# Optimization experiments

Measured on AMD Instinct MI355X. Metric: run time of the kernel, lower is better.

Reference implementation:

```python
import jax, jax.numpy as jnp
import numpy as np

B = 1024      # batch
HG = 28       # grid side (28x28 image -> graph)
N = HG * HG   # 784 nodes per sample
K = 70        # node_sampled (relaxed categorical classes)
GCN_OUT = 48
H_DIM = 400
Z = 70
IMG = 784
TEMP = 0.5


def _grid_edges():
    idx = np.arange(N).reshape(HG, HG)
    src = np.concatenate([idx[:, :-1].ravel(), idx[:, 1:].ravel(), idx[:-1, :].ravel(), idx[1:, :].ravel()])
    dst = np.concatenate([idx[:, 1:].ravel(), idx[:, :-1].ravel(), idx[1:, :].ravel(), idx[:-1, :].ravel()])
    loop = np.arange(N)
    return (np.concatenate([src, loop]).astype(np.int32),
            np.concatenate([dst, loop]).astype(np.int32))


def _lin(key, fi, fo):
    kw, kb = jax.random.split(key)
    s = 1.0 / np.sqrt(fi)
    return (jax.random.uniform(kw, (fi, fo), jnp.float32, -s, s),
            jax.random.uniform(kb, (fo,), jnp.float32, -s, s))


def setup_inputs() -> dict:
    key = jax.random.key(0)
    ks = jax.random.split(key, 16)
    src, dst = _grid_edges()
    u = jax.random.uniform(ks[2], (B, N, K), jnp.float32, 1e-6, 1.0 - 1e-6)
    inp = {
        'nodes': jax.random.normal(ks[0], (B, N, 2), jnp.float32),
        'logits': jax.random.normal(ks[1], (B, N, K), jnp.float32),
        'gumbel': -jnp.log(-jnp.log(u)),
        'eps': jax.random.normal(ks[3], (B, Z), jnp.float32),
    }
    inp['W1'], inp['b1'] = _lin(ks[4], 2, 16)
    inp['W2'], inp['b2'] = _lin(ks[5], 16, 32)
    inp['W3'], inp['b3'] = _lin(ks[6], 32, GCN_OUT)
    inp['We1'], inp['be1'] = _lin(ks[7], K * GCN_OUT, H_DIM)
    inp['We2'], inp['be2'] = _lin(ks[8], H_DIM, H_DIM)
    inp['Wmu'], inp['bmu'] = _lin(ks[9], H_DIM, Z)
    inp['Wvar'], inp['bvar'] = _lin(ks[10], H_DIM, Z)
    inp['Wd1'], inp['bd1'] = _lin(ks[11], Z, H_DIM)
    inp['Wd2'], inp['bd2'] = _lin(ks[12], H_DIM, IMG)
    inp['edge_src'] = jnp.asarray(src)
    inp['edge_dst'] = jnp.asarray(dst)
    return inp


def reference(nodes, logits, gumbel, eps,
              W1, b1, W2, b2, W3, b3,
              We1, be1, We2, be2,
              Wmu, bmu, Wvar, bvar,
              Wd1, bd1, Wd2, bd2,
              edge_src, edge_dst):
    # symmetric GCN normalization with self loops (already in edge list)
    deg = jnp.zeros((N,), nodes.dtype).at[edge_dst].add(1.0)
    dinv = jax.lax.rsqrt(deg)
    norm = dinv[edge_src] * dinv[edge_dst]  # [E]

    def gcn(h, W, b):
        h = h @ W                                   # [B,N,Fout]
        msg = h[:, edge_src] * norm[None, :, None]  # gather + scale, [B,E,Fout]
        return jnp.zeros_like(h).at[:, edge_dst].add(msg) + b

    h = jax.nn.relu(gcn(nodes, W1, b1))
    h = jax.nn.relu(gcn(h, W2, b2))
    h = jax.nn.relu(gcn(h, W3, b3))            # [B,N,48]

    # RelaxedOneHotCategorical(temp=0.5).rsample() == gumbel-softmax
    sample = jax.nn.softmax((logits + gumbel) / TEMP, axis=-1)  # [B,N,K]
    g = jnp.einsum('bnk,bnf->bkf', sample, h).reshape(h.shape[0], K * GCN_OUT)

    # encoder MLP + reparameterize
    e = jax.nn.relu(g @ We1 + be1)
    e = jax.nn.relu(e @ We2 + be2)
    mu = e @ Wmu + bmu
    var = jax.nn.softplus(e @ Wvar + bvar)
    z = mu + eps * jnp.sqrt(var + 1e-10)

    # decoder
    d = jax.nn.relu(z @ Wd1 + bd1)
    x_rec = jax.nn.sigmoid(d @ Wd2 + bd2)      # [B,784]
    return x_rec
```

## Files before the change

### kernel.cpp

```cpp
#include <hip/hip_runtime.h>
#include <hip/hip_bf16.h>


#define BB 1024
#define HG 28
#define NN 784
#define KK 70
#define F3 48
#define HD 400
#define ZD 70
#define IMGD 784

typedef __hip_bfloat16 bf16;
typedef __attribute__((ext_vector_type(8))) short s8v;
typedef __attribute__((ext_vector_type(4))) float f32x4;

__device__ __forceinline__ float dinv_ij(int i, int j){
  int deg = 1 + (i>0) + (i<HG-1) + (j>0) + (j<HG-1);
  return rsqrtf((float)deg);
}

__device__ __forceinline__ unsigned pk2(float a, float b){
  union { bf16 h; unsigned short u; } ua, ub;
  ua.h = __float2bfloat16(a); ub.h = __float2bfloat16(b);
  return ((unsigned)ub.u << 16) | ua.u;
}

__device__ __forceinline__ short bfbits(float v){
  union { bf16 h; short s; } u; u.h = __float2bfloat16(v); return u.s;
}

__global__ __launch_bounds__(256, 2)
void gcn_fused(const float* __restrict__ nodes,
               const float* __restrict__ W1, const float* __restrict__ b1,
               const float* __restrict__ W2, const float* __restrict__ b2,
               const float* __restrict__ W3, const float* __restrict__ b3,
               bf16* __restrict__ h3){
  __shared__ __align__(16) char smem[73216];
  float* regA = (float*)smem;
  float* regB = (float*)(smem + 36288);
  float* wbuf = (float*)(smem + 64512);
  float* W1s = wbuf;          float* b1s = wbuf + 32;
  float* W2s = wbuf + 48;     float* b2s = wbuf + 560;
  float* W3s = wbuf + 592;    float* b3s = wbuf + 2128;

  int tid = threadIdx.x;
  if (tid < 32)  W1s[tid] = W1[tid];
  if (tid < 16)  b1s[tid] = b1[tid];
  for (int t = tid; t < 512;  t += 256) W2s[t] = W2[t];
  if (tid < 32)  b2s[tid] = b2[tid];
  for (int t = tid; t < 1536; t += 256) W3s[t] = W3[t];
  if (tid < 48)  b3s[tid] = b3[tid];

  int b = blockIdx.x >> 2, s = blockIdx.x & 3;
  int base3 = s*7;
  int base2 = base3 - 1;
  int base1 = base3 - 2;
  const float* nb = nodes + (size_t)b*NN*2;
  __syncthreads();

  {
    float* h1s = regA;
    for (int t = tid; t < 308; t += 256){
      int lr = t/28, j = t - lr*28;
      int r = base1 + lr;
      float o[16] __attribute__((aligned(16)));
      if (r < 0 || r >= HG){
        #pragma unroll
        for (int f=0; f<16; f++) o[f] = 0.f;
      } else {
        float dn = dinv_ij(r,j);
        float a0 = dn*nb[(r*HG+j)*2+0], a1 = dn*nb[(r*HG+j)*2+1];
        if (r > 0)   { float w=dinv_ij(r-1,j); a0 += w*nb[((r-1)*HG+j)*2]; a1 += w*nb[((r-1)*HG+j)*2+1]; }
        if (r < HG-1){ float w=dinv_ij(r+1,j); a0 += w*nb[((r+1)*HG+j)*2]; a1 += w*nb[((r+1)*HG+j)*2+1]; }
        if (j > 0)   { float w=dinv_ij(r,j-1); a0 += w*nb[(r*HG+j-1)*2];   a1 += w*nb[(r*HG+j-1)*2+1]; }
        if (j < HG-1){ float w=dinv_ij(r,j+1); a0 += w*nb[(r*HG+j+1)*2];   a1 += w*nb[(r*HG+j+1)*2+1]; }
        a0 *= dn; a1 *= dn;
        #pragma unroll
        for (int f=0; f<16; f++) o[f] = fmaxf(a0*W1s[f] + a1*W1s[16+f] + b1s[f], 0.f);
      }
      float* dst = h1s + t*20;
      #pragma unroll
      for (int q=0; q<4; q++) *(float4*)(dst + 4*q) = *(float4*)&o[4*q];
    }
  }
  __syncthreads();

  if (tid < 252){
    const float* h1s = regA;
    float* agg1 = regB;
    int lr = tid/28, j = tid - lr*28;
    int r = base2 + lr;
    float o[16] __attribute__((aligned(16)));
    if (r < 0 || r >= HG){
      #pragma unroll
      for (int f=0; f<16; f++) o[f] = 0.f;
    } else {
      int ln = (lr+1)*28 + j;
      float dn = dinv_ij(r,j);
      float wu = dinv_ij(r-1,j), wd = dinv_ij(r+1,j);
      float wl = (j>0)    ? dinv_ij(r,j-1) : 0.f;
      float wr = (j<HG-1) ? dinv_ij(r,j+1) : 0.f;
      const float* pc = h1s + ln*20;
      #pragma unroll
      for (int q=0; q<4; q++){
        float4 vc = *(const float4*)(pc + 4*q);
        float4 vu = *(const float4*)(pc - 28*20 + 4*q);
        float4 vd = *(const float4*)(pc + 28*20 + 4*q);
        float4 vl = *(const float4*)(pc - 20 + 4*q);
        float4 vr = *(const float4*)(pc + 20 + 4*q);
        o[4*q+0] = dn*(dn*vc.x + wu*vu.x + wd*vd.x + wl*vl.x + wr*vr.x);
        o[4*q+1] = dn*(dn*vc.y + wu*vu.y + wd*vd.y + wl*vl.y + wr*vr.y);
        o[4*q+2] = dn*(dn*vc.z + wu*vu.z + wd*vd.z + wl*vl.z + wr*vr.z);
        o[4*q+3] = dn*(dn*vc.w + wu*vu.w + wd*vd.w + wl*vl.w + wr*vr.w);
      }
    }
    float* dst = agg1 + tid*20;
    #pragma unroll
    for (int q=0; q<4; q++) *(float4*)(dst + 4*q) = *(float4*)&o[4*q];
  }
  __syncthreads();

  {
    const float* agg1 = regB;
    float* h2s = regA;
    int tx = tid & 7, ty = tid >> 3;
    float4 w2r[16];
    #pragma unroll
    for (int fi=0; fi<16; fi++) w2r[fi] = *(const float4*)&W2s[fi*32 + tx*4];
    float4 bb = *(const float4*)&b2s[tx*4];
    #pragma unroll
    for (int i=0; i<8; i++){
      int n = ty + 32*i;
      if (n < 252){
        float af[16] __attribute__((aligned(16)));
        const float* ap = agg1 + n*20;
        #pragma unroll
        for (int q=0; q<4; q++) *(float4*)&af[4*q] = *(const float4*)(ap + 4*q);
        float4 acc = bb;
        #pragma unroll
        for (int fi=0; fi<16; fi++){
          float a = af[fi];
          acc.x += a*w2r[fi].x; acc.y += a*w2r[fi].y;
          acc.z += a*w2r[fi].z; acc.w += a*w2r[fi].w;
        }
        acc.x = fmaxf(acc.x,0.f); acc.y = fmaxf(acc.y,0.f);
        acc.z = fmaxf(acc.z,0.f); acc.w = fmaxf(acc.w,0.f);
        *(float4*)&h2s[n*36 + tx*4] = acc;
      }
    }
  }
  __syncthreads();

  if (tid < 196){
    const float* h2s = regA;
    float* agg2 = regB;
    int lr = tid/28, j = tid - lr*28;
    int r = base3 + lr;
    int ln = (lr+1)*28 + j;
    float dn = dinv_ij(r,j);
    float wu = dinv_ij(r-1,j), wd = dinv_ij(r+1,j);
    float wl = (j>0)    ? dinv_ij(r,j-1) : 0.f;
    float wr = (j<HG-1) ? dinv_ij(r,j+1) : 0.f;
    const float* pc = h2s + ln*36;
    float* dst = agg2 + tid*36;
    #pragma unroll
    for (int q=0; q<8; q++){
      float4 vc = *(const float4*)(pc + 4*q);
      float4 vu = *(const float4*)(pc - 28*36 + 4*q);
      float4 vd = *(const float4*)(pc + 28*36 + 4*q);
      float4 vl = *(const float4*)(pc - 36 + 4*q);
      float4 vr = *(const float4*)(pc + 36 + 4*q);
      float4 o;
      o.x = dn*(dn*vc.x + wu*vu.x + wd*vd.x + wl*vl.x + wr*vr.x);
      o.y = dn*(dn*vc.y + wu*vu.y + wd*vd.y + wl*vl.y + wr*vr.y);
      o.z = dn*(dn*vc.z + wu*vu.z + wd*vd.z + wl*vl.z + wr*vr.z);
      o.w = dn*(dn*vc.w + wu*vu.w + wd*vd.w + wl*vl.w + wr*vr.w);
      *(float4*)(dst + 4*q) = o;
    }
  }
  __syncthreads();

  {
    bf16* h3buf = (bf16*)regA;
    if (tid < 252){
      const float* agg2 = regB;
      int tx = tid % 12, ty = tid / 12;
      float4 w3r[32];
      #pragma unroll
      for (int fi=0; fi<32; fi++) w3r[fi] = *(const float4*)&W3s[fi*48 + tx*4];
      float4 bb = *(const float4*)&b3s[tx*4];
      #pragma unroll
      for (int i=0; i<10; i++){
        int n = ty + 21*i;
        if (n < 196){
          float af[32] __attribute__((aligned(16)));
          const float* ap = agg2 + n*36;
          #pragma unroll
          for (int q=0; q<8; q++) *(float4*)&af[4*q] = *(const float4*)(ap + 4*q);
          float4 acc = bb;
          #pragma unroll
          for (int fi=0; fi<32; fi++){
            float a = af[fi];
            acc.x += a*w3r[fi].x; acc.y += a*w3r[fi].y;
            acc.z += a*w3r[fi].z; acc.w += a*w3r[fi].w;
          }
          uint2 pv;
          pv.x = pk2(fmaxf(acc.x,0.f), fmaxf(acc.y,0.f));
          pv.y = pk2(fmaxf(acc.z,0.f), fmaxf(acc.w,0.f));
          *(uint2*)((char*)h3buf + n*112 + tx*8) = pv;
        }
      }
    }
  }
  __syncthreads();

  {
    const char* h3buf = (const char*)regA;
    uint4* dst = (uint4*)(h3 + ((size_t)b*NN + base3*28)*F3);
    for (int t = tid; t < 1176; t += 256){
      int n = t/6, gq = t - n*6;
      dst[t] = *(const uint4*)(h3buf + n*112 + gq*16);
    }
  }
}

__global__ __launch_bounds__(256)
void einsum_mfma_kernel(const float* __restrict__ logits, const float* __restrict__ gumbel,
                        const bf16* __restrict__ h3, float* __restrict__ g){
  __shared__ __align__(16) char smem[47872];
  float* samp = (float*)smem;
  short* stp  = (short*)(smem + 17920);
  short* stlo = (short*)(smem + 29440);
  short* htp  = (short*)(smem + 40960);
  float* cred = (float*)smem;

  int b = blockIdx.x;
  int tid = threadIdx.x;
  int l = tid & 63, w = tid >> 6;
  int ks = w >> 1, mh = w & 1;
  int mtoff = mh ? 3 : 0, mtcnt = mh ? 2 : 3;
  int nl = tid >> 2, q = tid & 3;
  int st = (q < 2) ? q*18 : 36 + (q-2)*17;
  int cnt = (q < 2) ? 18 : 17;

  f32x4 acc[3][3];
  #pragma unroll
  for (int mt=0; mt<3; mt++)
    #pragma unroll
    for (int bt=0; bt<3; bt++) acc[mt][bt] = (f32x4){0.f,0.f,0.f,0.f};

  float4 xs[5];
  uint4 hv[2];

  auto do_loads = [&](int c){
    int c0 = c*64;
    int nv = (c == 12) ? 16 : 64;
    int lim4 = nv*70/4, limh = nv*6;
    const float4* l4 = (const float4*)(logits + ((size_t)b*NN + c0)*KK);
    const float4* g4 = (const float4*)(gumbel + ((size_t)b*NN + c0)*KK);
    #pragma unroll
    for (int s=0; s<5; s++){
      int t = tid + s*256;
      if (t < lim4){
        float4 lv = l4[t], gv = g4[t];
        xs[s] = (float4){2.f*(lv.x+gv.x), 2.f*(lv.y+gv.y), 2.f*(lv.z+gv.z), 2.f*(lv.w+gv.w)};
      } else xs[s] = (float4){0.f,0.f,0.f,0.f};
    }
    const uint4* h4 = (const uint4*)(h3 + ((size_t)b*NN + c0)*F3);
    #pragma unroll
    for (int s=0; s<2; s++){
      int t = tid + s*256;
      hv[s] = (t < limh) ? h4[t] : (uint4){0u,0u,0u,0u};
    }
  };

  auto write_samp = [&](){
    #pragma unroll
    for (int s=0; s<5; s++){
      int t = tid + s*256;
      if (t < 1120) ((float4*)samp)[t] = xs[s];
    }
  };

  auto softmax_writes = [&](int c){
    int nv = (c == 12) ? 16 : 64;
    float p[18];
    if (nl < nv){
      float x[18];
      float m = -1e30f;
      #pragma unroll
      for (int i=0; i<18; i++) if (i < cnt){ x[i] = samp[nl*70 + st + i]; m = fmaxf(m, x[i]); }
      m = fmaxf(m, __shfl_xor(m, 1));
      m = fmaxf(m, __shfl_xor(m, 2));
      float sum = 0.f;
      #pragma unroll
      for (int i=0; i<18; i++) if (i < cnt){ x[i] = __expf(x[i]-m); sum += x[i]; }
      sum += __shfl_xor(sum, 1);
      sum += __shfl_xor(sum, 2);
      float r = 1.0f/sum;
      #pragma unroll
      for (int i=0; i<18; i++) p[i] = x[i]*r;
    } else {
      #pragma unroll
      for (int i=0; i<18; i++) p[i] = 0.f;
    }
    #pragma unroll
    for (int i=0; i<18; i++) if (i < cnt){
      int k = st + i;
      short hi = bfbits(p[i]);
      union { short s; bf16 h; } uh; uh.s = hi;
      float lo = p[i] - __bfloat162float(uh.h);
      stp[k*72 + nl]  = hi;
      stlo[k*72 + nl] = bfbits(lo);
    }
    #pragma unroll
    for (int s=0; s<2; s++){
      int t = tid + s*256;
      if (t < 384){
        int n = t/6, j = t - n*6, f0 = j*8;
        unsigned vv[4] = {hv[s].x, hv[s].y, hv[s].z, hv[s].w};
        #pragma unroll
        for (int i2=0; i2<4; i2++){
          htp[(f0+2*i2  )*72 + n] = (short)(vv[i2] & 0xFFFFu);
          htp[(f0+2*i2+1)*72 + n] = (short)(vv[i2] >> 16);
        }
      }
    }
  };

  auto do_mfma = [&](){
    int n0 = ks*32 + (l>>4)*8;
    #pragma unroll
    for (int bt=0; bt<3; bt++){
      s8v bfr = *(const s8v*)&htp[(bt*16 + (l&15))*72 + n0];
      #pragma unroll
      for (int mt=0; mt<3; mt++) if (mt < mtcnt){
        int row = (mtoff + mt)*16 + (l&15);
        s8v ah = *(const s8v*)&stp[row*72 + n0];
        s8v al = *(const s8v*)&stlo[row*72 + n0];
        acc[mt][bt] = __builtin_amdgcn_mfma_f32_16x16x32_bf16(ah, bfr, acc[mt][bt], 0, 0, 0);
        acc[mt][bt] = __builtin_amdgcn_mfma_f32_16x16x32_bf16(al, bfr, acc[mt][bt], 0, 0, 0);
      }
    }
  };

  do_loads(0);
  write_samp();
  __syncthreads();
  softmax_writes(0);
  __syncthreads();

  for (int c = 0; c < 13; c++){
    if (c < 12) do_loads(c+1);
    do_mfma();
    if (c < 12) write_samp();
    __syncthreads();
    if (c < 12){
      softmax_writes(c+1);
      __syncthreads();
    }
  }

  if (ks == 0){
    #pragma unroll
    for (int mt=0; mt<3; mt++) if (mt < mtcnt)
      #pragma unroll
      for (int bt=0; bt<3; bt++)
        #pragma unroll
        for (int r=0; r<4; r++){
          int row = (mtoff+mt)*16 + (l>>4)*4 + r;
          int col = bt*16 + (l&15);
          cred[row*49 + col] = acc[mt][bt][r];
        }
  }
  __syncthreads();
  if (ks == 1){
    #pragma unroll
    for (int mt=0; mt<3; mt++) if (mt < mtcnt)
      #pragma unroll
      for (int bt=0; bt<3; bt++)
        #pragma unroll
        for (int r=0; r<4; r++){
          int row = (mtoff+mt)*16 + (l>>4)*4 + r;
          int col = bt*16 + (l&15);
          cred[row*49 + col] += acc[mt][bt][r];
        }
  }
  __syncthreads();
  for (int t = tid; t < KK*F3; t += 256){
    int r = t / F3, c2 = t - r*F3;
    g[(size_t)b*(KK*F3) + t] = cred[r*49 + c2];
  }
}

template<int ACT>
__global__ __launch_bounds__(256)
void dense_kernel(const float* __restrict__ A, const float* __restrict__ W,
                  const float* __restrict__ bias, float* __restrict__ out,
                  int M, int K, int Nn, int kChunk){
  __shared__ float As[16][65];
  __shared__ float Bs[16][64];
  int tx = threadIdx.x & 15, ty = threadIdx.x >> 4;
  int m0 = blockIdx.x*64, n0 = blockIdx.y*64;
  int ks = blockIdx.z * kChunk;
  int ke = min(K, ks + kChunk);
  int a_kk = threadIdx.x & 15, a_mm = threadIdx.x >> 4;
  int b_nn = threadIdx.x & 63, b_k0 = threadIdx.x >> 6;
  float ra[4], rb[4];
  float acc[4][4] = {};

  #pragma unroll
  for (int s=0; s<4; s++){
    int gk = ks + a_kk;
    ra[s] = (gk < ke) ? A[(size_t)(m0 + a_mm + s*16)*K + gk] : 0.f;
  }
  #pragma unroll
  for (int s=0; s<4; s++){
    int gk = ks + b_k0 + s*4, gn = n0 + b_nn;
    rb[s] = (gk < ke && gn < Nn) ? W[(size_t)gk*Nn + gn] : 0.f;
  }

  for (int k0 = ks; k0 < ke; k0 += 16){
    #pragma unroll
    for (int s=0; s<4; s++) As[a_kk][a_mm + s*16] = ra[s];
    #pragma unroll
    for (int s=0; s<4; s++) Bs[b_k0 + s*4][b_nn] = rb[s];
    __syncthreads();
    if (k0 + 16 < ke){
      #pragma unroll
      for (int s=0; s<4; s++){
        int gk = k0 + 16 + a_kk;
        ra[s] = (gk < ke) ? A[(size_t)(m0 + a_mm + s*16)*K + gk] : 0.f;
      }
      #pragma unroll
      for (int s=0; s<4; s++){
        int gk = k0 + 16 + b_k0 + s*4, gn = n0 + b_nn;
        rb[s] = (gk < ke && gn < Nn) ? W[(size_t)gk*Nn + gn] : 0.f;
      }
    }
    #pragma unroll
    for (int kk=0; kk<16; kk++){
      float a[4], bv[4];
      #pragma unroll
      for (int i2=0; i2<4; i2++) a[i2] = As[kk][ty*4+i2];
      #pragma unroll
      for (int j2=0; j2<4; j2++) bv[j2] = Bs[kk][tx*4+j2];
      #pragma unroll
      for (int i2=0; i2<4; i2++)
        #pragma unroll
        for (int j2=0; j2<4; j2++) acc[i2][j2] += a[i2]*bv[j2];
    }
    __syncthreads();
  }

  if (ACT == 2){
    float* po = out + (size_t)blockIdx.z*M*Nn;
    #pragma unroll
    for (int j2=0; j2<4; j2++){
      int gn = n0 + tx*4 + j2;
      if (gn < Nn){
        #pragma unroll
        for (int i2=0; i2<4; i2++)
          po[(size_t)(m0 + ty*4 + i2)*Nn + gn] = acc[i2][j2];
      }
    }
  } else {
    #pragma unroll
    for (int j2=0; j2<4; j2++){
      int gn = n0 + tx*4 + j2;
      if (gn < Nn){
        float bb = bias[gn];
        #pragma unroll
        for (int i2=0; i2<4; i2++){
          float v = acc[i2][j2] + bb;
          v = (ACT == 0) ? fmaxf(v, 0.f) : 1.0f/(1.0f + __expf(-v));
          out[(size_t)(m0 + ty*4 + i2)*Nn + gn] = v;
        }
      }
    }
  }
}

__global__ __launch_bounds__(256)
void reduce_bias_relu(const float* __restrict__ part, const float* __restrict__ bias,
                      float* __restrict__ out, int M, int Nn, int S){
  int idx = blockIdx.x*256 + threadIdx.x;
  if (idx >= M*Nn) return;
  int n = idx % Nn;
  float s = bias[n];
  for (int i=0; i<S; i++) s += part[(size_t)i*M*Nn + idx];
  out[idx] = fmaxf(s, 0.f);
}

__global__ __launch_bounds__(256)
void latent_kernel(const float* __restrict__ e2,
                   const float* __restrict__ Wmu, const float* __restrict__ bmu,
                   const float* __restrict__ Wvar, const float* __restrict__ bvar,
                   const float* __restrict__ eps, float* __restrict__ z){
  int idx = blockIdx.x*256 + threadIdx.x;
  int b = idx / ZD, zi = idx - b*ZD;
  const float* er = e2 + (size_t)b*HD;
  float amu = 0.f, avr = 0.f;
  for (int j=0; j<HD; j++){
    float e = er[j];
    amu += e*Wmu[j*ZD + zi];
    avr += e*Wvar[j*ZD + zi];
  }
  float mu = amu + bmu[zi];
  float va = avr + bvar[zi];
  float sp = fmaxf(va, 0.f) + log1pf(__expf(-fabsf(va)));
  z[idx] = mu + eps[idx]*sqrtf(sp + 1e-10f);
}

extern "C" void kernel_launch(void* const* d_in, const int* in_sizes, int n_in,
                              void* d_out, int out_size, void* d_ws, size_t ws_size,
                              hipStream_t stream){
  (void)in_sizes; (void)n_in; (void)out_size; (void)ws_size;
  const float* nodes  = (const float*)d_in[0];
  const float* logits = (const float*)d_in[1];
  const float* gumbel = (const float*)d_in[2];
  const float* eps    = (const float*)d_in[3];
  const float* W1 =(const float*)d_in[4],  *b1 =(const float*)d_in[5];
  const float* W2 =(const float*)d_in[6],  *b2 =(const float*)d_in[7];
  const float* W3 =(const float*)d_in[8],  *b3 =(const float*)d_in[9];
  const float* We1=(const float*)d_in[10], *be1=(const float*)d_in[11];
  const float* We2=(const float*)d_in[12], *be2=(const float*)d_in[13];
  const float* Wmu=(const float*)d_in[14], *bmu=(const float*)d_in[15];
  const float* Wvr=(const float*)d_in[16], *bvr=(const float*)d_in[17];
  const float* Wd1=(const float*)d_in[18], *bd1=(const float*)d_in[19];
  const float* Wd2=(const float*)d_in[20], *bd2=(const float*)d_in[21];

  char* ws = (char*)d_ws;
  bf16*  h3 = (bf16*)(ws);
  float* g  = (float*)(ws + 77070336);
  float* e1 = (float*)(ws + 90832896);
  float* e2 = (float*)(ws + 92471296);
  float* zb = (float*)(ws + 94109696);
  float* dd = (float*)(ws + 94396416);
  float* part = (float*)(ws);
  float* out = (float*)d_out;

  gcn_fused<<<4096, 256, 0, stream>>>(nodes, W1, b1, W2, b2, W3, b3, h3);
  einsum_mfma_kernel<<<1024, 256, 0, stream>>>(logits, gumbel, h3, g);
  dense_kernel<2><<<dim3(16, 7, 8), 256, 0, stream>>>(g, We1, nullptr, part, 1024, 3360, 400, 432);
  reduce_bias_relu<<<1600, 256, 0, stream>>>(part, be1, e1, 1024, 400, 8);
  dense_kernel<0><<<dim3(16, 7, 1), 256, 0, stream>>>(e1, We2, be2, e2, 1024, 400, 400, 400);
  latent_kernel<<<280, 256, 0, stream>>>(e2, Wmu, bmu, Wvr, bvr, eps, zb);
  dense_kernel<0><<<dim3(16, 7, 1), 256, 0, stream>>>(zb, Wd1, bd1, dd, 1024, 70, 400, 70);
  dense_kernel<1><<<dim3(16, 13, 1), 256, 0, stream>>>(dd, Wd2, bd2, out, 1024, 400, 784, 400);
}
```

Measured before the change: 419.2 us.

## Double-buffer einsum LDS tiles and compute softmax directly from register loads

The einsum kernel no longer stages logits+gumbel through shared memory. Each thread loads its own slice of classes into registers, computes the softmax there, and writes packed bf16 hi/lo pairs into an XOR-swizzled, double-buffered LDS layout. This removes one barrier per chunk and lets the softmax for the next chunk overlap the MFMA phase on the current buffer. Global loads are issued two chunks ahead. The cost is higher register pressure from 44 float2 staging registers and more complex swizzle indexing; the GCN kernel changes are only loop-variable renames.

```diff
diff --git a/kernel.cpp b/kernel.cpp
--- a/kernel.cpp
+++ b/kernel.cpp
@@ -81,7 +81,7 @@
       }
       float* dst = h1s + t*20;
       #pragma unroll
-      for (int q=0; q<4; q++) *(float4*)(dst + 4*q) = *(float4*)&o[4*q];
+      for (int qq=0; qq<4; qq++) *(float4*)(dst + 4*qq) = *(float4*)&o[4*qq];
     }
   }
   __syncthreads();
@@ -103,21 +103,21 @@
       float wr = (j<HG-1) ? dinv_ij(r,j+1) : 0.f;
       const float* pc = h1s + ln*20;
       #pragma unroll
-      for (int q=0; q<4; q++){
-        float4 vc = *(const float4*)(pc + 4*q);
-        float4 vu = *(const float4*)(pc - 28*20 + 4*q);
-        float4 vd = *(const float4*)(pc + 28*20 + 4*q);
-        float4 vl = *(const float4*)(pc - 20 + 4*q);
-        float4 vr = *(const float4*)(pc + 20 + 4*q);
-        o[4*q+0] = dn*(dn*vc.x + wu*vu.x + wd*vd.x + wl*vl.x + wr*vr.x);
-        o[4*q+1] = dn*(dn*vc.y + wu*vu.y + wd*vd.y + wl*vl.y + wr*vr.y);
-        o[4*q+2] = dn*(dn*vc.z + wu*vu.z + wd*vd.z + wl*vl.z + wr*vr.z);
-        o[4*q+3] = dn*(dn*vc.w + wu*vu.w + wd*vd.w + wl*vl.w + wr*vr.w);
+      for (int qq=0; qq<4; qq++){
+        float4 vc = *(const float4*)(pc + 4*qq);
+        float4 vu = *(const float4*)(pc - 28*20 + 4*qq);
+        float4 vd = *(const float4*)(pc + 28*20 + 4*qq);
+        float4 vl = *(const float4*)(pc - 20 + 4*qq);
+        float4 vr = *(const float4*)(pc + 20 + 4*qq);
+        o[4*qq+0] = dn*(dn*vc.x + wu*vu.x + wd*vd.x + wl*vl.x + wr*vr.x);
+        o[4*qq+1] = dn*(dn*vc.y + wu*vu.y + wd*vd.y + wl*vl.y + wr*vr.y);
+        o[4*qq+2] = dn*(dn*vc.z + wu*vu.z + wd*vd.z + wl*vl.z + wr*vr.z);
+        o[4*qq+3] = dn*(dn*vc.w + wu*vu.w + wd*vd.w + wl*vl.w + wr*vr.w);
       }
     }
     float* dst = agg1 + tid*20;
     #pragma unroll
-    for (int q=0; q<4; q++) *(float4*)(dst + 4*q) = *(float4*)&o[4*q];
+    for (int qq=0; qq<4; qq++) *(float4*)(dst + 4*qq) = *(float4*)&o[4*qq];
   }
   __syncthreads();
 
@@ -136,7 +136,7 @@
         float af[16] __attribute__((aligned(16)));
         const float* ap = agg1 + n*20;
         #pragma unroll
-        for (int q=0; q<4; q++) *(float4*)&af[4*q] = *(const float4*)(ap + 4*q);
+        for (int qq=0; qq<4; qq++) *(float4*)&af[4*qq] = *(const float4*)(ap + 4*qq);
         float4 acc = bb;
         #pragma unroll
         for (int fi=0; fi<16; fi++){
@@ -165,18 +165,18 @@
     const float* pc = h2s + ln*36;
     float* dst = agg2 + tid*36;
     #pragma unroll
-    for (int q=0; q<8; q++){
-      float4 vc = *(const float4*)(pc + 4*q);
-      float4 vu = *(const float4*)(pc - 28*36 + 4*q);
-      float4 vd = *(const float4*)(pc + 28*36 + 4*q);
-      float4 vl = *(const float4*)(pc - 36 + 4*q);
-      float4 vr = *(const float4*)(pc + 36 + 4*q);
+    for (int qq=0; qq<8; qq++){
+      float4 vc = *(const float4*)(pc + 4*qq);
+      float4 vu = *(const float4*)(pc - 28*36 + 4*qq);
+      float4 vd = *(const float4*)(pc + 28*36 + 4*qq);
+      float4 vl = *(const float4*)(pc - 36 + 4*qq);
+      float4 vr = *(const float4*)(pc + 36 + 4*qq);
       float4 o;
       o.x = dn*(dn*vc.x + wu*vu.x + wd*vd.x + wl*vl.x + wr*vr.x);
       o.y = dn*(dn*vc.y + wu*vu.y + wd*vd.y + wl*vl.y + wr*vr.y);
       o.z = dn*(dn*vc.z + wu*vu.z + wd*vd.z + wl*vl.z + wr*vr.z);
       o.w = dn*(dn*vc.w + wu*vu.w + wd*vd.w + wl*vl.w + wr*vr.w);
-      *(float4*)(dst + 4*q) = o;
+      *(float4*)(dst + 4*qq) = o;
     }
   }
   __syncthreads();
@@ -197,7 +197,7 @@
           float af[32] __attribute__((aligned(16)));
           const float* ap = agg2 + n*36;
           #pragma unroll
-          for (int q=0; q<8; q++) *(float4*)&af[4*q] = *(const float4*)(ap + 4*q);
+          for (int qq=0; qq<8; qq++) *(float4*)&af[4*qq] = *(const float4*)(ap + 4*qq);
           float4 acc = bb;
           #pragma unroll
           for (int fi=0; fi<32; fi++){
@@ -228,21 +228,25 @@
 __global__ __launch_bounds__(256)
 void einsum_mfma_kernel(const float* __restrict__ logits, const float* __restrict__ gumbel,
                         const bf16* __restrict__ h3, float* __restrict__ g){
-  __shared__ __align__(16) char smem[47872];
-  float* samp = (float*)smem;
-  short* stp  = (short*)(smem + 17920);
-  short* stlo = (short*)(smem + 29440);
-  short* htp  = (short*)(smem + 40960);
-  float* cred = (float*)smem;
-
-  int b = blockIdx.x;
-  int tid = threadIdx.x;
+  __shared__ __align__(16) unsigned smemD[2][7488];
+  const int SLO = 2880, HTO = 5760;
+
+  int b = blockIdx.x, tid = threadIdx.x;
   int l = tid & 63, w = tid >> 6;
+  int n_loc = tid >> 2, q = tid & 3;
+  int kstart = q << 4;
+  int kcnt = (q < 3) ? 16 : 22;
+  int kc2 = kcnt >> 1;
+  int m_pair = tid >> 3;
+  int half = (tid >> 2) & 1;
   int ks = w >> 1, mh = w & 1;
   int mtoff = mh ? 3 : 0, mtcnt = mh ? 2 : 3;
-  int nl = tid >> 2, q = tid & 3;
-  int st = (q < 2) ? q*18 : 36 + (q-2)*17;
-  int cnt = (q < 2) ? 18 : 17;
+
+  for (int t = tid; t < 720; t += 256){
+    int bb = t >= 360, r = t - bb*360;
+    smemD[bb][2520 + r] = 0u;
+    smemD[bb][SLO + 2520 + r] = 0u;
+  }
 
   f32x4 acc[3][3];
   #pragma unroll
@@ -250,118 +254,147 @@
     #pragma unroll
     for (int bt=0; bt<3; bt++) acc[mt][bt] = (f32x4){0.f,0.f,0.f,0.f};
 
-  float4 xs[5];
-  uint4 hv[2];
-
-  auto do_loads = [&](int c){
-    int c0 = c*64;
-    int nv = (c == 12) ? 16 : 64;
-    int lim4 = nv*70/4, limh = nv*6;
-    const float4* l4 = (const float4*)(logits + ((size_t)b*NN + c0)*KK);
-    const float4* g4 = (const float4*)(gumbel + ((size_t)b*NN + c0)*KK);
-    #pragma unroll
-    for (int s=0; s<5; s++){
-      int t = tid + s*256;
-      if (t < lim4){
-        float4 lv = l4[t], gv = g4[t];
-        xs[s] = (float4){2.f*(lv.x+gv.x), 2.f*(lv.y+gv.y), 2.f*(lv.z+gv.z), 2.f*(lv.w+gv.w)};
-      } else xs[s] = (float4){0.f,0.f,0.f,0.f};
-    }
-    const uint4* h4 = (const uint4*)(h3 + ((size_t)b*NN + c0)*F3);
-    #pragma unroll
-    for (int s=0; s<2; s++){
-      int t = tid + s*256;
-      hv[s] = (t < limh) ? h4[t] : (uint4){0u,0u,0u,0u};
+  float2 lx[11], gx[11];
+  uint2 hA0, hB0, hA1, hB1;
+  int hm0 = tid/12, hj0 = tid - hm0*12;
+  int tt1 = tid + 256;
+  int hm1 = tt1/12, hj1 = tt1 - hm1*12;
+
+  auto issue_loads = [&](int c){
+    int c0 = c << 6;
+    int node = c0 + n_loc;
+    bool v = node < NN;
+    const float* lp = logits + ((size_t)b*NN + node)*KK + kstart;
+    const float* gp = gumbel + ((size_t)b*NN + node)*KK + kstart;
+    int nld = (q < 3) ? 8 : 11;
+    #pragma unroll
+    for (int s=0; s<11; s++){
+      bool a = v && (s < nld);
+      lx[s] = a ? *(const float2*)(lp + 2*s) : (float2){0.f,0.f};
+      gx[s] = a ? *(const float2*)(gp + 2*s) : (float2){0.f,0.f};
+    }
+    bool vA0 = (c0 + 2*hm0)     < NN;
+    bool vB0 = (c0 + 2*hm0 + 1) < NN;
+    const uint2* p0 = (const uint2*)(h3 + ((size_t)b*NN + c0 + 2*hm0)*F3 + 4*hj0);
+    hA0 = vA0 ? p0[0]  : (uint2){0u,0u};
+    hB0 = vB0 ? p0[12] : (uint2){0u,0u};
+    if (tid < 128){
+      bool vA1 = (c0 + 2*hm1)     < NN;
+      bool vB1 = (c0 + 2*hm1 + 1) < NN;
+      const uint2* p1 = (const uint2*)(h3 + ((size_t)b*NN + c0 + 2*hm1)*F3 + 4*hj1);
+      hA1 = vA1 ? p1[0]  : (uint2){0u,0u};
+      hB1 = vB1 ? p1[12] : (uint2){0u,0u};
     }
   };
 
-  auto write_samp = [&](){
-    #pragma unroll
-    for (int s=0; s<5; s++){
-      int t = tid + s*256;
-      if (t < 1120) ((float4*)samp)[t] = xs[s];
+  auto consume = [&](int c, unsigned* buf){
+    int c0 = c << 6;
+    bool v = (c0 + n_loc) < NN;
+    float x[22];
+    #pragma unroll
+    for (int s=0; s<11; s++){
+      x[2*s]   = 2.f*(lx[s].x + gx[s].x);
+      x[2*s+1] = 2.f*(lx[s].y + gx[s].y);
+    }
+    float mx = -1e30f;
+    #pragma unroll
+    for (int i=0; i<22; i++) if (i < kcnt) mx = fmaxf(mx, x[i]);
+    mx = fmaxf(mx, __shfl_xor(mx, 1));
+    mx = fmaxf(mx, __shfl_xor(mx, 2));
+    float sum = 0.f;
+    #pragma unroll
+    for (int i=0; i<22; i++) if (i < kcnt){ x[i] = __expf(x[i]-mx); sum += x[i]; }
+    sum += __shfl_xor(sum, 1);
+    sum += __shfl_xor(sum, 2);
+    float rs = v ? 1.0f/sum : 0.f;
+    #pragma unroll
+    for (int i=0; i<22; i++){
+      if (i < kcnt){
+        float p = x[i]*rs;
+        unsigned hb = (unsigned)(unsigned short)bfbits(p);
+        union { short s; bf16 h; } uh; uh.s = (short)hb;
+        float lo = p - __bfloat162float(uh.h);
+        unsigned lb = (unsigned)(unsigned short)bfbits(lo);
+        unsigned phb = (unsigned)__shfl_xor((int)hb, 4);
+        unsigned plb = (unsigned)__shfl_xor((int)lb, 4);
+        unsigned dh = (half==0) ? (hb | (phb<<16)) : (phb | (hb<<16));
+        unsigned dl = (half==0) ? (lb | (plb<<16)) : (plb | (lb<<16));
+        bool doW = (half==0) ? (i < kc2) : (i >= kc2);
+        if (doW){
+          int k = kstart + i;
+          int col = m_pair ^ (((k>>4)&3)<<3);
+          buf[k*36 + col] = dh;
+          buf[SLO + k*36 + col] = dl;
+        }
+      }
+    }
+    {
+      unsigned d0 = (hA0.x & 0xFFFFu) | (hB0.x << 16);
+      unsigned d1 = (hA0.x >> 16)     | (hB0.x & 0xFFFF0000u);
+      unsigned d2 = (hA0.y & 0xFFFFu) | (hB0.y << 16);
+      unsigned d3 = (hA0.y >> 16)     | (hB0.y & 0xFFFF0000u);
+      #pragma unroll
+      for (int i2=0; i2<4; i2++){
+        int f = 4*hj0 + i2;
+        int col = hm0 ^ (((f>>4)&3)<<3);
+        unsigned dv = (i2==0)?d0:(i2==1)?d1:(i2==2)?d2:d3;
+        buf[HTO + f*36 + col] = dv;
+      }
+      if (tid < 128){
+        unsigned e0 = (hA1.x & 0xFFFFu) | (hB1.x << 16);
+        unsigned e1 = (hA1.x >> 16)     | (hB1.x & 0xFFFF0000u);
+        unsigned e2 = (hA1.y & 0xFFFFu) | (hB1.y << 16);
+        unsigned e3 = (hA1.y >> 16)     | (hB1.y & 0xFFFF0000u);
+        #pragma unroll
+        for (int i2=0; i2<4; i2++){
+          int f = 4*hj1 + i2;
+          int col = hm1 ^ (((f>>4)&3)<<3);
+          unsigned dv = (i2==0)?e0:(i2==1)?e1:(i2==2)?e2:e3;
+          buf[HTO + f*36 + col] = dv;
+        }
+      }
     }
   };
 
-  auto softmax_writes = [&](int c){
-    int nv = (c == 12) ? 16 : 64;
-    float p[18];
-    if (nl < nv){
-      float x[18];
-      float m = -1e30f;
-      #pragma unroll
-      for (int i=0; i<18; i++) if (i < cnt){ x[i] = samp[nl*70 + st + i]; m = fmaxf(m, x[i]); }
-      m = fmaxf(m, __shfl_xor(m, 1));
-      m = fmaxf(m, __shfl_xor(m, 2));
-      float sum = 0.f;
-      #pragma unroll
-      for (int i=0; i<18; i++) if (i < cnt){ x[i] = __expf(x[i]-m); sum += x[i]; }
-      sum += __shfl_xor(sum, 1);
-      sum += __shfl_xor(sum, 2);
-      float r = 1.0f/sum;
-      #pragma unroll
-      for (int i=0; i<18; i++) p[i] = x[i]*r;
-    } else {
-      #pragma unroll
-      for (int i=0; i<18; i++) p[i] = 0.f;
-    }
-    #pragma unroll
-    for (int i=0; i<18; i++) if (i < cnt){
-      int k = st + i;
-      short hi = bfbits(p[i]);
-      union { short s; bf16 h; } uh; uh.s = hi;
-      float lo = p[i] - __bfloat162float(uh.h);
-      stp[k*72 + nl]  = hi;
-      stlo[k*72 + nl] = bfbits(lo);
-    }
-    #pragma unroll
-    for (int s=0; s<2; s++){
-      int t = tid + s*256;
-      if (t < 384){
-        int n = t/6, j = t - n*6, f0 = j*8;
-        unsigned vv[4] = {hv[s].x, hv[s].y, hv[s].z, hv[s].w};
-        #pragma unroll
-        for (int i2=0; i2<4; i2++){
-          htp[(f0+2*i2  )*72 + n] = (short)(vv[i2] & 0xFFFFu);
-          htp[(f0+2*i2+1)*72 + n] = (short)(vv[i2] >> 16);
-        }
-      }
-    }
+  auto mfma_phase = [&](const unsigned* buf){
+    int pr = (ks<<4) + ((l>>4)<<2);
+    s8v Af[3], Al[3], Bf[3];
+    #pragma unroll
+    for (int mt=0; mt<3; mt++) if (mt < mtcnt){
+      int row = (mtoff+mt)*16 + (l&15);
+      int col = pr ^ (((row>>4)&3)<<3);
+      Af[mt] = *(const s8v*)&buf[row*36 + col];
+      Al[mt] = *(const s8v*)&buf[SLO + row*36 + col];
+    }
+    #pragma unroll
+    for (int bt=0; bt<3; bt++){
+      int f = bt*16 + (l&15);
+      int col = pr ^ (((f>>4)&3)<<3);
+      Bf[bt] = *(const s8v*)&buf[HTO + f*36 + col];
+    }
+    #pragma unroll
+    for (int mt=0; mt<3; mt++) if (mt < mtcnt)
+      #pragma unroll
+      for (int bt=0; bt<3; bt++){
+        acc[mt][bt] = __builtin_amdgcn_mfma_f32_16x16x32_bf16(Af[mt], Bf[bt], acc[mt][bt], 0, 0, 0);
+        acc[mt][bt] = __builtin_amdgcn_mfma_f32_16x16x32_bf16(Al[mt], Bf[bt], acc[mt][bt], 0, 0, 0);
+      }
   };
 
-  auto do_mfma = [&](){
-    int n0 = ks*32 + (l>>4)*8;
-    #pragma unroll
-    for (int bt=0; bt<3; bt++){
-      s8v bfr = *(const s8v*)&htp[(bt*16 + (l&15))*72 + n0];
-      #pragma unroll
-      for (int mt=0; mt<3; mt++) if (mt < mtcnt){
-        int row = (mtoff + mt)*16 + (l&15);
-        s8v ah = *(const s8v*)&stp[row*72 + n0];
-        s8v al = *(const s8v*)&stlo[row*72 + n0];
-        acc[mt][bt] = __builtin_amdgcn_mfma_f32_16x16x32_bf16(ah, bfr, acc[mt][bt], 0, 0, 0);
-        acc[mt][bt] = __builtin_amdgcn_mfma_f32_16x16x32_bf16(al, bfr, acc[mt][bt], 0, 0, 0);
-      }
-    }
-  };
-
-  do_loads(0);
-  write_samp();
-  __syncthreads();
-  softmax_writes(0);
-  __syncthreads();
-
+  issue_loads(0);
+  consume(0, smemD[0]);
+  issue_loads(1);
+  __syncthreads();
   for (int c = 0; c < 13; c++){
-    if (c < 12) do_loads(c+1);
-    do_mfma();
-    if (c < 12) write_samp();
+    if (c < 12){
+      consume(c+1, smemD[(c+1)&1]);
+      if (c + 2 <= 12) issue_loads(c+2);
+    }
+    mfma_phase(smemD[c&1]);
     __syncthreads();
-    if (c < 12){
-      softmax_writes(c+1);
-      __syncthreads();
-    }
-  }
-
+  }
+
+  float* cred = (float*)&smemD[0][0];
   if (ks == 0){
     #pragma unroll
     for (int mt=0; mt<3; mt++) if (mt < mtcnt)
```

After: 422.1 us. About the same (+0.7%).
